# Performance work log

Hardware: AMD Instinct MI355X
Metric: run time of the kernel (lower is better)

The kernel has to match this reference:

```python
import jax, jax.numpy as jnp
import numpy as np

B, C, L = 16, 256, 16384
M = C // 4  # mid_channels = in_channels // ratio (reduction=True)
LN_EPS = 1e-5


def setup_inputs() -> dict:
    key = jax.random.key(0)
    ks = jax.random.split(key, 8)
    s = 0.05
    return {
        "x": jax.random.normal(ks[0], (B, C, L), dtype=jnp.float32),
        "w_mask": jax.random.normal(ks[1], (C,), dtype=jnp.float32) * s,   # conv_mask weight (1,C,1) squeezed
        "b_mask": jax.random.normal(ks[2], (), dtype=jnp.float32) * s,
        "w1": jax.random.normal(ks[3], (M, C), dtype=jnp.float32) * s,      # conv1x1 C->M
        "b1": jax.random.normal(ks[4], (M,), dtype=jnp.float32) * s,
        "ln_g": jnp.ones((M,), dtype=jnp.float32),                           # LayerNorm([M,1]) weight
        "ln_b": jnp.zeros((M,), dtype=jnp.float32),
        "w2": jax.random.normal(ks[5], (C, M), dtype=jnp.float32) * s,      # conv1x1 M->C
        "b2": jax.random.normal(ks[6], (C,), dtype=jnp.float32) * s,
    }


def reference(x, w_mask, b_mask, w1, b1, ln_g, ln_b, w2, b2):
    # spatial attention pooling: conv_mask (1x1 conv C->1) + softmax over seq_len
    logits = jnp.einsum("bcl,c->bl", x, w_mask) + b_mask          # (B, L)
    attn = jax.nn.softmax(logits, axis=-1)                         # (B, L)
    ctx = jnp.einsum("bcl,bl->bc", x, attn)                        # (B, C)  == matmul pooling

    # channel_add_conv: conv1x1 -> LayerNorm([M,1]) -> ReLU -> conv1x1
    h = jnp.einsum("bc,mc->bm", ctx, w1) + b1                      # (B, M)
    mu = jnp.mean(h, axis=-1, keepdims=True)
    var = jnp.mean((h - mu) ** 2, axis=-1, keepdims=True)
    h = (h - mu) * jax.lax.rsqrt(var + LN_EPS) * ln_g + ln_b
    h = jax.nn.relu(h)
    add = jnp.einsum("bm,cm->bc", h, w2) + b2                      # (B, C)

    return x + add[:, :, None]                                     # broadcast over seq_len
```

## Files before the change

kernel.cpp:

```cpp
#include <hip/hip_runtime.h>
#include <math.h>

#define Bn 16
#define Cn 256
#define Ln 16384
#define Mn 64
#define LN_EPS 1e-5f
#define CHUNK 64
#define NCH (Ln / CHUNK)
#define XSTR 65

typedef float v4f __attribute__((ext_vector_type(4)));

__global__ __launch_bounds__(256) void k_pool(
        const float* __restrict__ x, const float* __restrict__ w_mask,
        const float* __restrict__ b_mask,
        float* __restrict__ ctxU,
        float* __restrict__ mz) {
    const int ch = blockIdx.x, b = blockIdx.y;
    const int t = threadIdx.x;
    __shared__ float xs[Cn * XSTR];
    __shared__ float wm_s[Cn];
    __shared__ float red2[4 * CHUNK];
    __shared__ float e_s[CHUNK];

    wm_s[t] = w_mask[t];

    const size_t xbase = (size_t)b * Cn * Ln + (size_t)ch * CHUNK;
    const int sub = t >> 4;
    const int f4 = t & 15;
    #pragma unroll
    for (int r = 0; r < 16; ++r) {
        const int c = r * 16 + sub;
        float4 v = *(const float4*)(x + xbase + (size_t)c * Ln + 4 * f4);
        float* dst = xs + c * XSTR + 4 * f4;
        dst[0] = v.x; dst[1] = v.y; dst[2] = v.z; dst[3] = v.w;
    }
    __syncthreads();

    const int wv = t >> 6, lane = t & 63;
    {
        float p = 0.f;
        #pragma unroll 8
        for (int k = 0; k < 64; ++k) {
            const int c = wv * 64 + k;
            p += xs[c * XSTR + lane] * wm_s[c];
        }
        red2[wv * CHUNK + lane] = p;
    }
    __syncthreads();
    if (t < 64) {
        const float logit = red2[t] + red2[64 + t] + red2[128 + t] + red2[192 + t]
                          + b_mask[0];
        float m = logit;
        for (int off = 32; off; off >>= 1) m = fmaxf(m, __shfl_xor(m, off, 64));
        const float e = expf(logit - m);
        e_s[t] = e;
        float z = e;
        for (int off = 32; off; off >>= 1) z += __shfl_xor(z, off, 64);
        if (t == 0) {
            mz[(b * NCH + ch) * 2 + 0] = m;
            mz[(b * NCH + ch) * 2 + 1] = z;
        }
    }
    __syncthreads();

    float acc = 0.f;
    #pragma unroll 8
    for (int l = 0; l < CHUNK; ++l)
        acc += xs[t * XSTR + l] * e_s[l];
    ctxU[((size_t)b * NCH + ch) * Cn + t] = acc;
}

__global__ void k_comb_mlp(const float* __restrict__ ctxU, const float* __restrict__ mz,
                           const float* __restrict__ w1, const float* __restrict__ b1,
                           const float* __restrict__ ln_g, const float* __restrict__ ln_b,
                           const float* __restrict__ w2, const float* __restrict__ b2,
                           float* __restrict__ add) {
    const int b = blockIdx.x;
    const int t = threadIdx.x;
    __shared__ float s_sc[NCH];
    __shared__ float s_red[8];
    __shared__ float ctx_s[Cn];
    __shared__ float h_s[Mn];

    const float mt = mz[(b * NCH + t) * 2 + 0];
    const float zt = mz[(b * NCH + t) * 2 + 1];
    float M = mt;
    for (int off = 32; off; off >>= 1) M = fmaxf(M, __shfl_xor(M, off, 64));
    if ((t & 63) == 0) s_red[t >> 6] = M;
    __syncthreads();
    M = fmaxf(fmaxf(s_red[0], s_red[1]), fmaxf(s_red[2], s_red[3]));
    const float sc = expf(mt - M);
    float zw = zt * sc;
    for (int off = 32; off; off >>= 1) zw += __shfl_xor(zw, off, 64);
    if ((t & 63) == 0) s_red[4 + (t >> 6)] = zw;
    __syncthreads();
    const float Z = s_red[4] + s_red[5] + s_red[6] + s_red[7];
    s_sc[t] = sc / Z;
    __syncthreads();

    float s = 0.f;
    for (int chk = 0; chk < NCH; ++chk)
        s += ctxU[((size_t)b * NCH + chk) * Cn + t] * s_sc[chk];
    ctx_s[t] = s;
    __syncthreads();

    const int m4 = t >> 2, j = t & 3;
    float hp = 0.f;
    for (int c = j; c < Cn; c += 4) hp += ctx_s[c] * w1[m4 * Cn + c];
    hp += __shfl_xor(hp, 1, 64);
    hp += __shfl_xor(hp, 2, 64);
    if (j == 0) h_s[m4] = hp + b1[m4];
    __syncthreads();

    if (t < 64) {
        float h = h_s[t];
        float mu = h;
        for (int off = 32; off; off >>= 1) mu += __shfl_xor(mu, off, 64);
        mu *= (1.f / 64.f);
        const float d = h - mu;
        float var = d * d;
        for (int off = 32; off; off >>= 1) var += __shfl_xor(var, off, 64);
        var *= (1.f / 64.f);
        h = d * rsqrtf(var + LN_EPS) * ln_g[t] + ln_b[t];
        h_s[t] = fmaxf(h, 0.f);
    }
    __syncthreads();

    float a = b2[t];
    #pragma unroll
    for (int mm = 0; mm < Mn; ++mm) a += h_s[mm] * w2[t * Mn + mm];
    add[b * Cn + t] = a;
}

__global__ void k_out(const float* __restrict__ x, const float* __restrict__ add,
                      float* __restrict__ out) {
    const int bc = blockIdx.y;
    const float a = add[bc];
    const size_t base = (size_t)bc * Ln + (size_t)blockIdx.x * 4096;
    const float4* xi = (const float4*)(x + base);
    v4f* xo = (v4f*)(out + base);
    const int t = threadIdx.x;
    #pragma unroll
    for (int k = 0; k < 4; ++k) {
        float4 v = xi[k * 256 + t];
        v4f o = {v.x + a, v.y + a, v.z + a, v.w + a};
        __builtin_nontemporal_store(o, xo + k * 256 + t);
    }
}

extern "C" void kernel_launch(void* const* d_in, const int* in_sizes, int n_in,
                              void* d_out, int out_size, void* d_ws, size_t ws_size,
                              hipStream_t stream) {
    const float* x      = (const float*)d_in[0];
    const float* w_mask = (const float*)d_in[1];
    const float* b_mask = (const float*)d_in[2];
    const float* w1     = (const float*)d_in[3];
    const float* b1     = (const float*)d_in[4];
    const float* ln_g   = (const float*)d_in[5];
    const float* ln_b   = (const float*)d_in[6];
    const float* w2     = (const float*)d_in[7];
    const float* b2     = (const float*)d_in[8];
    float* out = (float*)d_out;

    float* ws   = (float*)d_ws;
    float* ctxU = ws;
    float* mz   = ctxU + (size_t)Bn * NCH * Cn;
    float* add  = mz + (size_t)Bn * NCH * 2;

    k_pool<<<dim3(NCH, Bn), 256, 0, stream>>>(x, w_mask, b_mask, ctxU, mz);
    k_comb_mlp<<<Bn, 256, 0, stream>>>(ctxU, mz, w1, b1, ln_g, ln_b, w2, b2, add);
    k_out<<<dim3(4, Bn * Cn), 256, 0, stream>>>(x, add, out);
}
```

Baseline: 142.0 us.

## Halve pooling chunk size and split combine stage into parallel scale/ctx/MLP kernels

Pooling chunks shrink from 64 to 32 positions, so k_pool launches twice as many blocks with half the shared memory each, which should raise occupancy. The combine step is split into three kernels: one computes the per-chunk softmax scales, one reduces the partial contexts across 256 blocks instead of 16, and one runs the small MLP. The goal is to replace a 16-block serial loop over chunks with a wider reduction. The cost is twice as much partial-context data written and read, plus two extra kernel launches.

```diff
diff --git a/kernel.cpp b/kernel.cpp
--- a/kernel.cpp
+++ b/kernel.cpp
@@ -6,9 +6,9 @@
 #define Ln 16384
 #define Mn 64
 #define LN_EPS 1e-5f
-#define CHUNK 64
+#define CHUNK 32
 #define NCH (Ln / CHUNK)
-#define XSTR 65
+#define XSTR 33
 
 typedef float v4f __attribute__((ext_vector_type(4)));
 
@@ -21,43 +21,44 @@
     const int t = threadIdx.x;
     __shared__ float xs[Cn * XSTR];
     __shared__ float wm_s[Cn];
-    __shared__ float red2[4 * CHUNK];
+    __shared__ float red2[8 * CHUNK];
     __shared__ float e_s[CHUNK];
 
     wm_s[t] = w_mask[t];
 
     const size_t xbase = (size_t)b * Cn * Ln + (size_t)ch * CHUNK;
-    const int sub = t >> 4;
-    const int f4 = t & 15;
+    const int c0 = t >> 3;
+    const int f4 = t & 7;
     #pragma unroll
-    for (int r = 0; r < 16; ++r) {
-        const int c = r * 16 + sub;
+    for (int r = 0; r < 8; ++r) {
+        const int c = r * 32 + c0;
         float4 v = *(const float4*)(x + xbase + (size_t)c * Ln + 4 * f4);
         float* dst = xs + c * XSTR + 4 * f4;
         dst[0] = v.x; dst[1] = v.y; dst[2] = v.z; dst[3] = v.w;
     }
     __syncthreads();
 
-    const int wv = t >> 6, lane = t & 63;
+    const int hw = t >> 5, lA = t & 31;
     {
         float p = 0.f;
         #pragma unroll 8
-        for (int k = 0; k < 64; ++k) {
-            const int c = wv * 64 + k;
-            p += xs[c * XSTR + lane] * wm_s[c];
+        for (int k = 0; k < 32; ++k) {
+            const int c = hw * 32 + k;
+            p += xs[c * XSTR + lA] * wm_s[c];
         }
-        red2[wv * CHUNK + lane] = p;
-    }
-    __syncthreads();
-    if (t < 64) {
-        const float logit = red2[t] + red2[64 + t] + red2[128 + t] + red2[192 + t]
-                          + b_mask[0];
+        red2[hw * CHUNK + lA] = p;
+    }
+    __syncthreads();
+    if (t < CHUNK) {
+        float logit = b_mask[0];
+        #pragma unroll
+        for (int j = 0; j < 8; ++j) logit += red2[j * CHUNK + t];
         float m = logit;
-        for (int off = 32; off; off >>= 1) m = fmaxf(m, __shfl_xor(m, off, 64));
+        for (int off = 16; off; off >>= 1) m = fmaxf(m, __shfl_xor(m, off, 32));
         const float e = expf(logit - m);
         e_s[t] = e;
         float z = e;
-        for (int off = 32; off; off >>= 1) z += __shfl_xor(z, off, 64);
+        for (int off = 16; off; off >>= 1) z += __shfl_xor(z, off, 32);
         if (t == 0) {
             mz[(b * NCH + ch) * 2 + 0] = m;
             mz[(b * NCH + ch) * 2 + 1] = z;
@@ -72,38 +73,63 @@
     ctxU[((size_t)b * NCH + ch) * Cn + t] = acc;
 }
 
-__global__ void k_comb_mlp(const float* __restrict__ ctxU, const float* __restrict__ mz,
-                           const float* __restrict__ w1, const float* __restrict__ b1,
-                           const float* __restrict__ ln_g, const float* __restrict__ ln_b,
-                           const float* __restrict__ w2, const float* __restrict__ b2,
-                           float* __restrict__ add) {
+__global__ void k_scale(const float* __restrict__ mz, float* __restrict__ s_sc) {
     const int b = blockIdx.x;
     const int t = threadIdx.x;
-    __shared__ float s_sc[NCH];
-    __shared__ float s_red[8];
+    __shared__ float red[8];
+    const float m0 = mz[(b * NCH + t) * 2],       z0 = mz[(b * NCH + t) * 2 + 1];
+    const float m1 = mz[(b * NCH + 256 + t) * 2], z1 = mz[(b * NCH + 256 + t) * 2 + 1];
+    float m = fmaxf(m0, m1);
+    for (int off = 32; off; off >>= 1) m = fmaxf(m, __shfl_xor(m, off, 64));
+    if ((t & 63) == 0) red[t >> 6] = m;
+    __syncthreads();
+    const float M = fmaxf(fmaxf(red[0], red[1]), fmaxf(red[2], red[3]));
+    float zw = z0 * expf(m0 - M) + z1 * expf(m1 - M);
+    for (int off = 32; off; off >>= 1) zw += __shfl_xor(zw, off, 64);
+    if ((t & 63) == 0) red[4 + (t >> 6)] = zw;
+    __syncthreads();
+    const float Z = red[4] + red[5] + red[6] + red[7];
+    s_sc[b * NCH + t]       = expf(m0 - M) / Z;
+    s_sc[b * NCH + 256 + t] = expf(m1 - M) / Z;
+}
+
+__global__ void k_ctx(const float* __restrict__ ctxU, const float* __restrict__ s_sc,
+                      float* __restrict__ ctx) {
+    const int cblk = blockIdx.x, b = blockIdx.y;
+    const int t = threadIdx.x;
+    __shared__ float sc_s[NCH];
+    __shared__ float red[256];
+    sc_s[t] = s_sc[b * NCH + t];
+    sc_s[256 + t] = s_sc[b * NCH + 256 + t];
+    __syncthreads();
+
+    const int cl = t & 15, chl = t >> 4;
+    const int c = cblk * 16 + cl;
+    float p = 0.f;
+    #pragma unroll 8
+    for (int j = 0; j < 32; ++j) {
+        const int chk = j * 16 + chl;
+        p += ctxU[((size_t)b * NCH + chk) * Cn + c] * sc_s[chk];
+    }
+    red[chl * 16 + cl] = p;
+    __syncthreads();
+    if (t < 16) {
+        float s = 0.f;
+        #pragma unroll
+        for (int j = 0; j < 16; ++j) s += red[j * 16 + t];
+        ctx[b * Cn + cblk * 16 + t] = s;
+    }
+}
+
+__global__ void k_mlp(const float* __restrict__ ctx, const float* __restrict__ w1,
+                      const float* __restrict__ b1, const float* __restrict__ ln_g,
+                      const float* __restrict__ ln_b, const float* __restrict__ w2,
+                      const float* __restrict__ b2, float* __restrict__ add) {
+    const int b = blockIdx.x;
+    const int t = threadIdx.x;
     __shared__ float ctx_s[Cn];
     __shared__ float h_s[Mn];
-
-    const float mt = mz[(b * NCH + t) * 2 + 0];
-    const float zt = mz[(b * NCH + t) * 2 + 1];
-    float M = mt;
-    for (int off = 32; off; off >>= 1) M = fmaxf(M, __shfl_xor(M, off, 64));
-    if ((t & 63) == 0) s_red[t >> 6] = M;
-    __syncthreads();
-    M = fmaxf(fmaxf(s_red[0], s_red[1]), fmaxf(s_red[2], s_red[3]));
-    const float sc = expf(mt - M);
-    float zw = zt * sc;
-    for (int off = 32; off; off >>= 1) zw += __shfl_xor(zw, off, 64);
-    if ((t & 63) == 0) s_red[4 + (t >> 6)] = zw;
-    __syncthreads();
-    const float Z = s_red[4] + s_red[5] + s_red[6] + s_red[7];
-    s_sc[t] = sc / Z;
-    __syncthreads();
-
-    float s = 0.f;
-    for (int chk = 0; chk < NCH; ++chk)
-        s += ctxU[((size_t)b * NCH + chk) * Cn + t] * s_sc[chk];
-    ctx_s[t] = s;
+    ctx_s[t] = ctx[b * Cn + t];
     __syncthreads();
 
     const int m4 = t >> 2, j = t & 3;
@@ -167,9 +193,13 @@
     float* ws   = (float*)d_ws;
     float* ctxU = ws;
     float* mz   = ctxU + (size_t)Bn * NCH * Cn;
-    float* add  = mz + (size_t)Bn * NCH * 2;
+    float* s_sc = mz + (size_t)Bn * NCH * 2;
+    float* ctx  = s_sc + (size_t)Bn * NCH;
+    float* add  = ctx + (size_t)Bn * Cn;
 
     k_pool<<<dim3(NCH, Bn), 256, 0, stream>>>(x, w_mask, b_mask, ctxU, mz);
-    k_comb_mlp<<<Bn, 256, 0, stream>>>(ctxU, mz, w1, b1, ln_g, ln_b, w2, b2, add);
+    k_scale<<<Bn, 256, 0, stream>>>(mz, s_sc);
+    k_ctx<<<dim3(Cn / 16, Bn), 256, 0, stream>>>(ctxU, s_sc, ctx);
+    k_mlp<<<Bn, 256, 0, stream>>>(ctx, w1, b1, ln_g, ln_b, w2, b2, add);
     k_out<<<dim3(4, Bn * Cn), 256, 0, stream>>>(x, add, out);
 }
```

Result: no change. 142.7 us (+0.5%).
